# Performance work log

Hardware: AMD Instinct MI355X
Metric: run time of the kernel (lower is better)

## Reference

```python
import jax, jax.numpy as jnp
import numpy as np

B, S, E, A = 4, 2048, 1024, 1024

def setup_inputs() -> dict:
    key = jax.random.key(0)
    ks = jax.random.split(key, 6)
    scale = 1.0 / np.sqrt(E)
    return {
        "query": jax.random.normal(ks[0], (B, S, E), jnp.float32),
        "key": jax.random.normal(ks[1], (B, S, E), jnp.float32),
        "value": jax.random.normal(ks[2], (B, S, E), jnp.float32),
        "Wq": jax.random.normal(ks[3], (E, A), jnp.float32) * scale,
        "bq": jnp.zeros((A,), jnp.float32),
        "Wk": jax.random.normal(ks[4], (E, A), jnp.float32) * scale,
        "bk": jnp.zeros((A,), jnp.float32),
        "Wv": jax.random.normal(ks[5], (E, A), jnp.float32) * scale,
        "bv": jnp.zeros((A,), jnp.float32),
    }

def reference(query, key, value, Wq, bq, Wk, bk, Wv, bv):
    # QKV linear projections: [B,S,E] @ [E,A] + [A]
    q = jnp.einsum("bse,ea->bsa", query, Wq) + bq
    k = jnp.einsum("bse,ea->bsa", key, Wk) + bk
    v = jnp.einsum("bse,ea->bsa", value, Wv) + bv
    # scaled dot-product attention (no mask, single head)
    inv_sqrt_d = 1.0 / jnp.sqrt(jnp.asarray(A, q.dtype))
    scores = jnp.einsum("bqa,bka->bqk", q, k) * inv_sqrt_d  # [B,S,S]
    probs = jax.nn.softmax(scores, axis=-1)
    return jnp.einsum("bqk,bka->bqa", probs, v)
```

## Files before the change

kernel.cpp:

```cpp
#include <hip/hip_runtime.h>

typedef unsigned short u16;
typedef __attribute__((ext_vector_type(4))) float f32x4;
typedef __attribute__((ext_vector_type(8))) short s16x8;
typedef __attribute__((ext_vector_type(8))) unsigned short u16x8;
typedef __attribute__((ext_vector_type(4))) unsigned short u16x4;

__device__ __forceinline__ u16 f2b(float x) {
  union { float f; unsigned u; } v; v.f = x;
  unsigned r = v.u + 0x7fffu + ((v.u >> 16) & 1u);
  return (u16)(r >> 16);
}
__device__ __forceinline__ float b2f(u16 x) {
  union { unsigned u; float f; } v; v.u = ((unsigned)x) << 16;
  return v.f;
}

__global__ __launch_bounds__(256) void cast3_f32_bf16(const float* __restrict__ s0,
                                                      const float* __restrict__ s1,
                                                      const float* __restrict__ s2,
                                                      u16* __restrict__ dst, long n4) {
  const float* src = (blockIdx.y == 0) ? s0 : ((blockIdx.y == 1) ? s1 : s2);
  long i = blockIdx.x * 256 + threadIdx.x;
  if (i >= n4) return;
  float4 f = ((const float4*)src)[i];
  u16x4 o;
  o.x = f2b(f.x); o.y = f2b(f.y); o.z = f2b(f.z); o.w = f2b(f.w);
  ((u16x4*)(dst + blockIdx.y * n4 * 4))[i] = o;
}

__global__ __launch_bounds__(256) void transpose_cast_w3(const float* __restrict__ w0,
                                                         const float* __restrict__ w1,
                                                         const float* __restrict__ w2,
                                                         u16* __restrict__ Wt, int E_, int A_) {
  __shared__ float tile[32][33];
  const float* W = (blockIdx.z == 0) ? w0 : ((blockIdx.z == 1) ? w1 : w2);
  u16* dst = Wt + (long)blockIdx.z * E_ * A_;
  int a0 = blockIdx.x * 32, e0 = blockIdx.y * 32;
  int tx = threadIdx.x & 31, ty = threadIdx.x >> 5;
  for (int i = ty; i < 32; i += 8) tile[i][tx] = W[(long)(e0 + i) * A_ + a0 + tx];
  __syncthreads();
  for (int i = ty; i < 32; i += 8) dst[(long)(a0 + i) * E_ + e0 + tx] = f2b(tile[tx][i]);
}

__global__ __launch_bounds__(256) void transpose_bf16_64(const u16* __restrict__ src,
                                                         u16* __restrict__ dst, int rows, int cols) {
  __shared__ u16 tile[64][68];
  long bo = (long)blockIdx.z * rows * cols;
  int c0 = blockIdx.x * 64, r0 = blockIdx.y * 64;
  int t = threadIdx.x;
  int tx = t & 15, ty = t >> 4;
  for (int i = ty; i < 64; i += 16) {
    u16x4 v = *(const u16x4*)(src + bo + (long)(r0 + i) * cols + c0 + tx * 4);
    *(u16x4*)(&tile[i][tx * 4]) = v;
  }
  __syncthreads();
  for (int i = ty; i < 64; i += 16) {
    u16x4 o;
    o.x = tile[tx * 4 + 0][i];
    o.y = tile[tx * 4 + 1][i];
    o.z = tile[tx * 4 + 2][i];
    o.w = tile[tx * 4 + 3][i];
    *(u16x4*)(dst + bo + (long)(c0 + i) * rows + r0 + tx * 4) = o;
  }
}

template<bool OUT_BF16>
__global__ __launch_bounds__(256)
void gemm_bt(const u16* __restrict__ Ag, const u16* __restrict__ Bg,
             const float* __restrict__ b0, const float* __restrict__ b1,
             const float* __restrict__ b2, void* __restrict__ Cg,
             int M, int N, int K, float scale, long sA, long sB, long sC) {
  __shared__ u16 As[128 * 32];
  __shared__ u16 Bs[128 * 32];
  const int t = threadIdx.x;
  const int wave = t >> 6, lane = t & 63;
  const int quad = lane >> 4, l16 = lane & 15;
  const int wm = wave & 1, wn = wave >> 1;
  const int m0 = blockIdx.y * 128, n0 = blockIdx.x * 128;
  const int z = blockIdx.z;
  const float* bias = (z == 0) ? b0 : ((z == 1) ? b1 : b2);
  const long zA = (long)z * sA;
  const long zB = (long)z * sB;
  const long zC = (long)z * sC;

  const int ar = t >> 2, ac = (t & 3) * 8;
  const u16* Ap0 = Ag + zA + (long)(m0 + ar) * K + ac;
  const u16* Ap1 = Ag + zA + (long)(m0 + 64 + ar) * K + ac;
  const u16* Bp0 = Bg + zB + (long)(n0 + ar) * K + ac;
  const u16* Bp1 = Bg + zB + (long)(n0 + 64 + ar) * K + ac;
  u16* AsD0 = As + wave * 512;
  u16* AsD1 = As + 2048 + wave * 512;
  u16* BsD0 = Bs + wave * 512;
  u16* BsD1 = Bs + 2048 + wave * 512;

  f32x4 acc[4][4] = {};

  const u16* Ard = As + (wm * 64 + l16) * 32 + quad * 8;
  const u16* Brd = Bs + (wn * 64 + l16) * 32 + quad * 8;

  for (int k0 = 0; k0 < K; k0 += 32) {
    __builtin_amdgcn_global_load_lds(
        (const __attribute__((address_space(1))) unsigned int*)(Ap0 + k0),
        (__attribute__((address_space(3))) unsigned int*)AsD0, 16, 0, 0);
    __builtin_amdgcn_global_load_lds(
        (const __attribute__((address_space(1))) unsigned int*)(Ap1 + k0),
        (__attribute__((address_space(3))) unsigned int*)AsD1, 16, 0, 0);
    __builtin_amdgcn_global_load_lds(
        (const __attribute__((address_space(1))) unsigned int*)(Bp0 + k0),
        (__attribute__((address_space(3))) unsigned int*)BsD0, 16, 0, 0);
    __builtin_amdgcn_global_load_lds(
        (const __attribute__((address_space(1))) unsigned int*)(Bp1 + k0),
        (__attribute__((address_space(3))) unsigned int*)BsD1, 16, 0, 0);
    __syncthreads();

    s16x8 fa[4], fb[4];
#pragma unroll
    for (int i = 0; i < 4; i++) fa[i] = *(const s16x8*)(Ard + i * 512);
#pragma unroll
    for (int j = 0; j < 4; j++) fb[j] = *(const s16x8*)(Brd + j * 512);
#pragma unroll
    for (int i = 0; i < 4; i++)
#pragma unroll
      for (int j = 0; j < 4; j++)
        acc[i][j] = __builtin_amdgcn_mfma_f32_16x16x32_bf16(fa[i], fb[j], acc[i][j], 0, 0, 0);
    __syncthreads();
  }

  float bj[4];
#pragma unroll
  for (int j = 0; j < 4; j++) {
    int col = n0 + wn * 64 + j * 16 + l16;
    bj[j] = bias ? bias[col] : 0.0f;
  }
#pragma unroll
  for (int i = 0; i < 4; i++) {
#pragma unroll
    for (int r = 0; r < 4; r++) {
      long row = m0 + wm * 64 + i * 16 + quad * 4 + r;
      long ro = zC + row * (long)N;
#pragma unroll
      for (int j = 0; j < 4; j++) {
        int col = n0 + wn * 64 + j * 16 + l16;
        float v = acc[i][j][r] * scale + bj[j];
        if (OUT_BF16) ((u16*)Cg)[ro + col] = f2b(v);
        else          ((float*)Cg)[ro + col] = v;
      }
    }
  }
}

__device__ __forceinline__ float wred_max(float x) {
  for (int o = 32; o > 0; o >>= 1) x = fmaxf(x, __shfl_xor(x, o));
  return x;
}
__device__ __forceinline__ float wred_sum(float x) {
  for (int o = 32; o > 0; o >>= 1) x += __shfl_xor(x, o);
  return x;
}

__global__ __launch_bounds__(256) void softmax_rows_bf16(const u16* __restrict__ S,
                                                         u16* __restrict__ P, int ncols) {
  long row = blockIdx.x;
  const u16x8* s8 = (const u16x8*)(S + row * (long)ncols);
  int t = threadIdx.x;
  int wave = t >> 6, lane = t & 63;
  u16x8 a = s8[t];
  float f[8];
#pragma unroll
  for (int i = 0; i < 8; i++) f[i] = b2f(a[i]);
  float m = f[0];
#pragma unroll
  for (int i = 1; i < 8; i++) m = fmaxf(m, f[i]);
  m = wred_max(m);
  __shared__ float redm[4], reds[4];
  if (lane == 0) redm[wave] = m;
  __syncthreads();
  m = fmaxf(fmaxf(redm[0], redm[1]), fmaxf(redm[2], redm[3]));

  float e[8], s = 0.f;
#pragma unroll
  for (int i = 0; i < 8; i++) { e[i] = __expf(f[i] - m); s += e[i]; }
  s = wred_sum(s);
  if (lane == 0) reds[wave] = s;
  __syncthreads();
  s = reds[0] + reds[1] + reds[2] + reds[3];
  float inv = 1.0f / s;

  u16x8 o;
#pragma unroll
  for (int i = 0; i < 8; i++) o[i] = f2b(e[i] * inv);
  ((u16x8*)(P + row * (long)ncols))[t] = o;
}

extern "C" void kernel_launch(void* const* d_in, const int* in_sizes, int n_in,
                              void* d_out, int out_size, void* d_ws, size_t ws_size,
                              hipStream_t stream) {
  const float* query = (const float*)d_in[0];
  const float* key_  = (const float*)d_in[1];
  const float* value = (const float*)d_in[2];
  const float* Wq = (const float*)d_in[3];
  const float* bq = (const float*)d_in[4];
  const float* Wk = (const float*)d_in[5];
  const float* bk = (const float*)d_in[6];
  const float* Wv = (const float*)d_in[7];
  const float* bv = (const float*)d_in[8];

  constexpr int B = 4, S = 2048, E = 1024, A = 1024;
  constexpr long MB = 1024 * 1024;
  char* ws = (char*)d_ws;
  u16* Qb  = (u16*)(ws + 0 * MB);
  u16* Vt  = (u16*)(ws + 48 * MB);
  u16* P   = (u16*)(ws + 64 * MB);
  u16* Sc  = (u16*)(ws + 96 * MB);
  u16* Xq  = (u16*)(ws + 96 * MB);
  u16* WqT = (u16*)(ws + 144 * MB);
  u16* Kb  = (u16*)(ws + 16 * MB);

  const long n = (long)B * S * E;
  const long n4 = n / 4;
  dim3 blk(256);

  cast3_f32_bf16<<<dim3(n4 / 256, 3), blk, 0, stream>>>(query, key_, value, Xq, n4);

  transpose_cast_w3<<<dim3(A / 32, E / 32, 3), blk, 0, stream>>>(Wq, Wk, Wv, WqT, E, A);

  dim3 pg(A / 128, (B * S) / 128, 3);
  gemm_bt<true><<<pg, blk, 0, stream>>>(Xq, WqT, bq, bk, bv, Qb,
                                        B * S, A, E, 1.0f,
                                        (long)8 * MB, (long)1 * MB, (long)8 * MB);

  transpose_bf16_64<<<dim3(A / 64, S / 64, B), blk, 0, stream>>>((u16*)(ws + 32 * MB), Vt, S, A);

  dim3 sg(S / 128, S / 128, B);
  gemm_bt<true><<<sg, blk, 0, stream>>>(Qb, Kb, nullptr, nullptr, nullptr, Sc,
                                        S, S, A, 0.03125f,
                                        (long)S * A, (long)S * A, (long)S * S);

  softmax_rows_bf16<<<dim3(B * S), blk, 0, stream>>>(Sc, P, S);

  dim3 og(A / 128, S / 128, B);
  gemm_bt<false><<<og, blk, 0, stream>>>(P, Vt, nullptr, nullptr, nullptr, (float*)d_out,
                                         S, A, S, 1.0f,
                                         (long)S * S, (long)S * A, (long)S * A);
}
```

Baseline: 373.3 us.

## Fuse V transpose into projection epilogue and remap tiles for XCD locality

New measurement: 366.3 us. No clear change (-1.9%).

```diff
diff --git a/kernel.cpp b/kernel.cpp
--- a/kernel.cpp
+++ b/kernel.cpp
@@ -43,41 +43,29 @@
   for (int i = ty; i < 32; i += 8) dst[(long)(a0 + i) * E_ + e0 + tx] = f2b(tile[tx][i]);
 }
 
-__global__ __launch_bounds__(256) void transpose_bf16_64(const u16* __restrict__ src,
-                                                         u16* __restrict__ dst, int rows, int cols) {
-  __shared__ u16 tile[64][68];
-  long bo = (long)blockIdx.z * rows * cols;
-  int c0 = blockIdx.x * 64, r0 = blockIdx.y * 64;
-  int t = threadIdx.x;
-  int tx = t & 15, ty = t >> 4;
-  for (int i = ty; i < 64; i += 16) {
-    u16x4 v = *(const u16x4*)(src + bo + (long)(r0 + i) * cols + c0 + tx * 4);
-    *(u16x4*)(&tile[i][tx * 4]) = v;
-  }
-  __syncthreads();
-  for (int i = ty; i < 64; i += 16) {
-    u16x4 o;
-    o.x = tile[tx * 4 + 0][i];
-    o.y = tile[tx * 4 + 1][i];
-    o.z = tile[tx * 4 + 2][i];
-    o.w = tile[tx * 4 + 3][i];
-    *(u16x4*)(dst + bo + (long)(c0 + i) * rows + r0 + tx * 4) = o;
-  }
-}
-
 template<bool OUT_BF16>
 __global__ __launch_bounds__(256)
 void gemm_bt(const u16* __restrict__ Ag, const u16* __restrict__ Bg,
              const float* __restrict__ b0, const float* __restrict__ b1,
              const float* __restrict__ b2, void* __restrict__ Cg,
-             int M, int N, int K, float scale, long sA, long sB, long sC) {
+             int M, int N, int K, float scale, long sA, long sB, long sC,
+             int XM, int XN, u16* __restrict__ VtG, long vtB, int vtS) {
   __shared__ u16 As[128 * 32];
   __shared__ u16 Bs[128 * 32];
   const int t = threadIdx.x;
   const int wave = t >> 6, lane = t & 63;
   const int quad = lane >> 4, l16 = lane & 15;
   const int wm = wave & 1, wn = wave >> 1;
-  const int m0 = blockIdx.y * 128, n0 = blockIdx.x * 128;
+
+  const int gn = gridDim.x, gm = gridDim.y;
+  const int L = blockIdx.y * gn + blockIdx.x;
+  const int c = L & 7, tt = L >> 3;
+  const int sm = gm / XM, sn = gn / XN;
+  const int cm = c % XM, cn = c / XM;
+  const int tm = tt % sm, tn = tt / sm;
+  const int m0 = (cm * sm + tm) * 128;
+  const int n0 = (cn * sn + tn) * 128;
+
   const int z = blockIdx.z;
   const float* bias = (z == 0) ? b0 : ((z == 1) ? b1 : b2);
   const long zA = (long)z * sA;
@@ -133,18 +121,37 @@
     int col = n0 + wn * 64 + j * 16 + l16;
     bj[j] = bias ? bias[col] : 0.0f;
   }
-#pragma unroll
-  for (int i = 0; i < 4; i++) {
-#pragma unroll
-    for (int r = 0; r < 4; r++) {
-      long row = m0 + wm * 64 + i * 16 + quad * 4 + r;
-      long ro = zC + row * (long)N;
-#pragma unroll
-      for (int j = 0; j < 4; j++) {
-        int col = n0 + wn * 64 + j * 16 + l16;
-        float v = acc[i][j][r] * scale + bj[j];
-        if (OUT_BF16) ((u16*)Cg)[ro + col] = f2b(v);
-        else          ((float*)Cg)[ro + col] = v;
+
+  if (OUT_BF16 && VtG != nullptr && z == 2) {
+    const int b = m0 / (vtS);
+    const int smod = m0 % vtS;
+    u16* vbase = VtG + (long)b * vtB + smod;
+#pragma unroll
+    for (int i = 0; i < 4; i++) {
+#pragma unroll
+      for (int r = 0; r < 4; r++) {
+        int row = wm * 64 + i * 16 + quad * 4 + r;
+#pragma unroll
+        for (int j = 0; j < 4; j++) {
+          int col = n0 + wn * 64 + j * 16 + l16;
+          vbase[(long)col * vtS + row] = f2b(acc[i][j][r] * scale + bj[j]);
+        }
+      }
+    }
+  } else {
+#pragma unroll
+    for (int i = 0; i < 4; i++) {
+#pragma unroll
+      for (int r = 0; r < 4; r++) {
+        long row = m0 + wm * 64 + i * 16 + quad * 4 + r;
+        long ro = zC + row * (long)N;
+#pragma unroll
+        for (int j = 0; j < 4; j++) {
+          int col = n0 + wn * 64 + j * 16 + l16;
+          float v = acc[i][j][r] * scale + bj[j];
+          if (OUT_BF16) ((u16*)Cg)[ro + col] = f2b(v);
+          else          ((float*)Cg)[ro + col] = v;
+        }
       }
     }
   }
@@ -210,12 +217,12 @@
   constexpr long MB = 1024 * 1024;
   char* ws = (char*)d_ws;
   u16* Qb  = (u16*)(ws + 0 * MB);
+  u16* Kb  = (u16*)(ws + 16 * MB);
   u16* Vt  = (u16*)(ws + 48 * MB);
   u16* P   = (u16*)(ws + 64 * MB);
   u16* Sc  = (u16*)(ws + 96 * MB);
   u16* Xq  = (u16*)(ws + 96 * MB);
   u16* WqT = (u16*)(ws + 144 * MB);
-  u16* Kb  = (u16*)(ws + 16 * MB);
 
   const long n = (long)B * S * E;
   const long n4 = n / 4;
@@ -228,19 +235,20 @@
   dim3 pg(A / 128, (B * S) / 128, 3);
   gemm_bt<true><<<pg, blk, 0, stream>>>(Xq, WqT, bq, bk, bv, Qb,
                                         B * S, A, E, 1.0f,
-                                        (long)8 * MB, (long)1 * MB, (long)8 * MB);
-
-  transpose_bf16_64<<<dim3(A / 64, S / 64, B), blk, 0, stream>>>((u16*)(ws + 32 * MB), Vt, S, A);
+                                        (long)8 * MB, (long)1 * MB, (long)8 * MB,
+                                        8, 1, Vt, (long)A * S, S);
 
   dim3 sg(S / 128, S / 128, B);
   gemm_bt<true><<<sg, blk, 0, stream>>>(Qb, Kb, nullptr, nullptr, nullptr, Sc,
                                         S, S, A, 0.03125f,
-                                        (long)S * A, (long)S * A, (long)S * S);
+                                        (long)S * A, (long)S * A, (long)S * S,
+                                        4, 2, nullptr, 0, 0);
 
   softmax_rows_bf16<<<dim3(B * S), blk, 0, stream>>>(Sc, P, S);
 
   dim3 og(A / 128, S / 128, B);
   gemm_bt<false><<<og, blk, 0, stream>>>(P, Vt, nullptr, nullptr, nullptr, (float*)d_out,
                                          S, A, S, 1.0f,
-                                         (long)S * S, (long)S * A, (long)S * A);
-}
+                                         (long)S * S, (long)S * A, (long)S * A,
+                                         4, 2, nullptr, 0, 0);
+}
```
